# Performance work log

Hardware: AMD Instinct MI355X
Metric: run time of the kernel (lower is better)

## Reference

```python
import jax, jax.numpy as jnp
import numpy as np

N_NODES = 50000
N_EDGES = 800000
C_IN = 128
C_OUT = 64
C_HID = 2 * C_OUT  # 128


def setup_inputs() -> dict:
    key = jax.random.key(0)
    ks = jax.random.split(key, 8)
    x = jax.random.normal(ks[0], (N_NODES, C_IN), dtype=jnp.float32)
    edge_index = jax.random.randint(ks[1], (2, N_EDGES), 0, N_NODES, dtype=jnp.int64)
    s1 = 1.0 / np.sqrt(C_IN)
    s2 = 1.0 / np.sqrt(C_HID)
    s3 = 1.0 / np.sqrt(C_OUT)
    W1 = jax.random.uniform(ks[2], (C_IN, C_HID), jnp.float32, -s1, s1)
    b1 = jnp.zeros((C_HID,), jnp.float32)
    W2 = jax.random.uniform(ks[3], (C_HID, C_OUT), jnp.float32, -s2, s2)
    b2 = jnp.zeros((C_OUT,), jnp.float32)
    Wb = jax.random.uniform(ks[4], (1, C_OUT, C_OUT), jnp.float32, -s3, s3)
    bb = jax.random.uniform(ks[5], (1,), jnp.float32, -s3, s3)
    return {"x": x, "edge_index": edge_index, "W1": W1, "b1": b1,
            "W2": W2, "b2": b2, "Wb": Wb, "bb": bb}


def gcn_conv(x, W, b, src, dst, n_nodes):
    # PyG GCNConv: h = x @ W; add self-loops; symmetric normalization D^-1/2 (A+I) D^-1/2.
    h = x @ W  # [N, F]
    ones = jnp.ones((src.shape[0],), h.dtype)
    deg = jax.ops.segment_sum(ones, dst, num_segments=n_nodes) + 1.0  # +1 for self-loop
    dinv = jax.lax.rsqrt(deg)
    norm = dinv[src] * dinv[dst]  # [E]
    msgs = h[src] * norm[:, None]  # [E, F]
    agg = jax.ops.segment_sum(msgs, dst, num_segments=n_nodes)
    # self-loop contribution: norm_ii = 1/deg_i
    agg = agg + h * (1.0 / deg)[:, None]
    return agg + b


def reference(x, edge_index, W1, b1, W2, b2, Wb, bb):
    src = edge_index[0]
    dst = edge_index[1]
    n = x.shape[0]
    # encode
    h = jax.nn.relu(gcn_conv(x, W1, b1, src, dst, n))
    z = gcn_conv(h, W2, b2, src, dst, n)  # [N, C_OUT]
    # decode: bilinear on (z[src], z[dst]) -> sigmoid
    zs = z[src]  # [E, C_OUT]
    zd = z[dst]  # [E, C_OUT]
    logits = jnp.einsum('ec,ocd,ed->eo', zs, Wb, zd) + bb  # [E, 1]
    return jax.nn.sigmoid(logits)
```

## Files before the change

### kernel.cpp

```cpp
#include <hip/hip_runtime.h>
#include <hip/hip_bf16.h>


#define N_NODES 50000
#define BSH 7
#define BSZ 128
#define NBUCK ((N_NODES + BSZ - 1) / BSZ)
#define EPB 4096
#define CAP 3072
#define DSPLIT 4

typedef unsigned int u32;
typedef unsigned short u16;
typedef unsigned long long u64;

typedef __attribute__((ext_vector_type(8))) short bf16x8;
typedef __attribute__((ext_vector_type(4))) float f32x4;
union frag_u { bf16x8 f; u32 u[4]; uint4 v; };

__device__ __forceinline__ float bflo(u32 u) { return __uint_as_float(u << 16); }
__device__ __forceinline__ float bfhi(u32 u) { return __uint_as_float(u & 0xffff0000u); }
__device__ __forceinline__ u32 f2bf(float f) {
    u32 b = __float_as_uint(f);
    return (b + 0x7fffu + ((b >> 16) & 1u)) >> 16;
}
__device__ __forceinline__ u32 pack2(float a, float b) { return f2bf(a) | (f2bf(b) << 16); }

__global__ __launch_bounds__(256) void gemm1_scatter(
        const float* __restrict__ X, const float* __restrict__ W,
        u16* __restrict__ O, int n_rows, int gblk,
        const int* __restrict__ src, const int* __restrict__ dst,
        int* __restrict__ bcur, u64* __restrict__ pair, int E) {
    constexpr int K = 128, NOUT = 128;
    constexpr int KP = K + 8;
    constexpr int NT = NOUT / 16;
    constexpr int KS = K / 32;
    __shared__ __align__(16) char smem[NOUT * KP * 2 * sizeof(u16)];
    int t = threadIdx.x;

    if ((int)blockIdx.x < gblk) {
        u16* Wt_hi = (u16*)smem;
        u16* Wt_lo = Wt_hi + NOUT * KP;
        for (int i4 = t; i4 < K * NOUT / 4; i4 += 256) {
            int k = (i4 * 4) / NOUT;
            int n0 = (i4 * 4) % NOUT;
            float4 w4 = *(const float4*)&W[(size_t)k * NOUT + n0];
            float wv[4] = {w4.x, w4.y, w4.z, w4.w};
#pragma unroll
            for (int q = 0; q < 4; q++) {
                u32 hi = f2bf(wv[q]);
                u32 lo = f2bf(wv[q] - bflo(hi));
                Wt_hi[(n0 + q) * KP + k] = (u16)hi;
                Wt_lo[(n0 + q) * KP + k] = (u16)lo;
            }
        }
        __syncthreads();

        int wave = t >> 6;
        int lane = t & 63;
        int m16 = lane & 15;
        int quad = lane >> 4;
        int row0 = blockIdx.x * 128 + wave * 32;

        f32x4 acc[2][NT] = {};
        for (int ks = 0; ks < KS; ks++) {
            frag_u a_hi[2], a_lo[2];
#pragma unroll
            for (int mt = 0; mt < 2; mt++) {
                int row = row0 + mt * 16 + m16;
                row = row < n_rows ? row : n_rows - 1;
                const float* Xp = X + (size_t)row * K + ks * 32 + quad * 8;
                float4 x0 = *(const float4*)Xp;
                float4 x1 = *(const float4*)(Xp + 4);
                float xv[8] = {x0.x, x0.y, x0.z, x0.w, x1.x, x1.y, x1.z, x1.w};
#pragma unroll
                for (int p = 0; p < 4; p++) {
                    u32 h0 = f2bf(xv[2 * p]), h1 = f2bf(xv[2 * p + 1]);
                    a_hi[mt].u[p] = h0 | (h1 << 16);
                    a_lo[mt].u[p] = pack2(xv[2 * p] - bflo(h0), xv[2 * p + 1] - bflo(h1));
                }
            }
#pragma unroll
            for (int nt = 0; nt < NT; nt++) {
                int n = nt * 16 + m16;
                frag_u b_hi, b_lo;
                b_hi.v = *(const uint4*)&Wt_hi[n * KP + ks * 32 + quad * 8];
                b_lo.v = *(const uint4*)&Wt_lo[n * KP + ks * 32 + quad * 8];
#pragma unroll
                for (int mt = 0; mt < 2; mt++) {
                    acc[mt][nt] = __builtin_amdgcn_mfma_f32_16x16x32_bf16(a_hi[mt].f, b_hi.f, acc[mt][nt], 0, 0, 0);
                    acc[mt][nt] = __builtin_amdgcn_mfma_f32_16x16x32_bf16(a_hi[mt].f, b_lo.f, acc[mt][nt], 0, 0, 0);
                    acc[mt][nt] = __builtin_amdgcn_mfma_f32_16x16x32_bf16(a_lo[mt].f, b_hi.f, acc[mt][nt], 0, 0, 0);
                }
            }
        }
#pragma unroll
        for (int mt = 0; mt < 2; mt++)
#pragma unroll
            for (int nt = 0; nt < NT; nt++)
#pragma unroll
                for (int r = 0; r < 4; r++) {
                    int row = row0 + mt * 16 + quad * 4 + r;
                    if (row < n_rows)
                        O[(size_t)row * NOUT + nt * 16 + m16] = (u16)f2bf(acc[mt][nt][r]);
                }
    } else {
        int* hist = (int*)smem;
        for (int i = t; i < NBUCK; i += 256) hist[i] = 0;
        __syncthreads();
        int base = ((int)blockIdx.x - gblk) * EPB;
        int s_[16], d_[16];
#pragma unroll
        for (int it = 0; it < 16; it++) {
            int e = base + it * 256 + t;
            if (e < E) {
                s_[it] = src[e];
                d_[it] = dst[e];
                atomicAdd(&hist[d_[it] >> BSH], 1);
            } else {
                d_[it] = -1;
            }
        }
        __syncthreads();
        for (int b = t; b < NBUCK; b += 256) {
            int c = hist[b];
            hist[b] = c ? (b * CAP + atomicAdd(&bcur[b], c)) : 0;
        }
        __syncthreads();
#pragma unroll
        for (int it = 0; it < 16; it++) {
            if (d_[it] >= 0) {
                int b = d_[it] >> BSH;
                int off = atomicAdd(&hist[b], 1);
                int e = base + it * 256 + t;
                pair[off] = (u64)((u32)s_[it] | ((u32)(d_[it] & (BSZ - 1)) << 16))
                          | ((u64)(u32)e << 32);
            }
        }
    }
}

__global__ __launch_bounds__(256) void bucket_sort(u64* __restrict__ pair,
                                                   const int* __restrict__ bcur,
                                                   int* __restrict__ row_ptr,
                                                   int* __restrict__ col,
                                                   float* __restrict__ dinv,
                                                   float* __restrict__ inv, int n, int E) {
    __shared__ u64 prA[CAP];
    __shared__ u64 prB[CAP];
    __shared__ int ssum[256];
    __shared__ int histA[512];
    __shared__ int scA[512];
    __shared__ int cnt[BSZ];
    __shared__ int scn[BSZ];
    __shared__ int cur[BSZ];
    int t = threadIdx.x;
    int bucket = blockIdx.x;
    int base = bucket << BSH;
    int nn = min(BSZ, n - base);
    int accp = 0;
    for (int i = t; i < bucket; i += 256) accp += bcur[i];
    ssum[t] = accp;
    __syncthreads();
    for (int s = 128; s > 0; s >>= 1) {
        if (t < s) ssum[t] += ssum[t + s];
        __syncthreads();
    }
    int b0 = ssum[0];
    int cntE = bcur[bucket];
    int p0 = bucket * CAP;

    histA[t] = 0;
    histA[t + 256] = 0;
    __syncthreads();
    for (int j = t; j < cntE; j += 256) {
        u64 p = pair[p0 + j];
        prA[j] = p;
        atomicAdd(&histA[(int)(p & 0xffffu) >> BSH], 1);
    }
    __syncthreads();
    int h0 = histA[t], h1 = histA[t + 256];
    scA[t] = h0;
    scA[t + 256] = h1;
    __syncthreads();
    for (int off = 1; off < 512; off <<= 1) {
        int a0 = (t >= off) ? scA[t - off] : 0;
        int a1 = (t + 256 >= off) ? scA[t + 256 - off] : 0;
        __syncthreads();
        scA[t] += a0;
        scA[t + 256] += a1;
        __syncthreads();
    }
    histA[t] = scA[t] - h0;
    histA[t + 256] = scA[t + 256] - h1;
    __syncthreads();
    for (int j = t; j < cntE; j += 256) {
        u64 p = prA[j];
        int pos = atomicAdd(&histA[(int)(p & 0xffffu) >> BSH], 1);
        prB[pos] = p;
    }
    __syncthreads();
    for (int j = t; j < cntE; j += 256) pair[p0 + j] = prB[j];

    if (t < BSZ) cnt[t] = 0;
    __syncthreads();
    for (int j = t; j < cntE; j += 256)
        atomicAdd(&cnt[(int)((prB[j] >> 16) & (BSZ - 1))], 1);
    __syncthreads();
    if (t < BSZ) scn[t] = cnt[t];
    __syncthreads();
    for (int off = 1; off < BSZ; off <<= 1) {
        int a = (t < BSZ && t >= off) ? scn[t - off] : 0;
        __syncthreads();
        if (t < BSZ) scn[t] += a;
        __syncthreads();
    }
    if (t < nn) {
        int excl = b0 + scn[t] - cnt[t];
        row_ptr[base + t] = excl;
        cur[t] = excl;
        float d = (float)cnt[t] + 1.0f;
        dinv[base + t] = rsqrtf(d);
        inv[base + t] = 1.0f / d;
    }
    if (t == 0 && bucket == NBUCK - 1) row_ptr[n] = E;
    __syncthreads();
    for (int j = t; j < cntE; j += 256) {
        u64 p = prB[j];
        int ln = (int)((p >> 16) & (BSZ - 1));
        int pos = atomicAdd(&cur[ln], 1);
        col[pos] = (int)(p & 0xffffu);
    }
}

template <int K, int NOUT>
__global__ __launch_bounds__(256) void gemm_mfma_bf(const u16* __restrict__ Xv,
                                                    const float* __restrict__ W,
                                                    u16* __restrict__ O, int n_rows) {
    constexpr int KP = K + 8;
    constexpr int NT = NOUT / 16;
    constexpr int KS = K / 32;
    __shared__ __align__(16) u16 Wt_hi[NOUT * KP];
    __shared__ __align__(16) u16 Wt_lo[NOUT * KP];
    int t = threadIdx.x;
    for (int i4 = t; i4 < K * NOUT / 4; i4 += 256) {
        int k = (i4 * 4) / NOUT;
        int n0 = (i4 * 4) % NOUT;
        float4 w4 = *(const float4*)&W[(size_t)k * NOUT + n0];
        float wv[4] = {w4.x, w4.y, w4.z, w4.w};
#pragma unroll
        for (int q = 0; q < 4; q++) {
            u32 hi = f2bf(wv[q]);
            u32 lo = f2bf(wv[q] - bflo(hi));
            Wt_hi[(n0 + q) * KP + k] = (u16)hi;
            Wt_lo[(n0 + q) * KP + k] = (u16)lo;
        }
    }
    __syncthreads();

    int wave = t >> 6;
    int lane = t & 63;
    int m16 = lane & 15;
    int quad = lane >> 4;
    int row0 = blockIdx.x * 128 + wave * 32;

    f32x4 acc[2][NT] = {};
    for (int ks = 0; ks < KS; ks++) {
        frag_u a_hi[2];
#pragma unroll
        for (int mt = 0; mt < 2; mt++) {
            int row = row0 + mt * 16 + m16;
            row = row < n_rows ? row : n_rows - 1;
            a_hi[mt].v = *(const uint4*)(Xv + (size_t)row * K + ks * 32 + quad * 8);
        }
#pragma unroll
        for (int nt = 0; nt < NT; nt++) {
            int n = nt * 16 + m16;
            frag_u b_hi, b_lo;
            b_hi.v = *(const uint4*)&Wt_hi[n * KP + ks * 32 + quad * 8];
            b_lo.v = *(const uint4*)&Wt_lo[n * KP + ks * 32 + quad * 8];
#pragma unroll
            for (int mt = 0; mt < 2; mt++) {
                acc[mt][nt] = __builtin_amdgcn_mfma_f32_16x16x32_bf16(a_hi[mt].f, b_hi.f, acc[mt][nt], 0, 0, 0);
                acc[mt][nt] = __builtin_amdgcn_mfma_f32_16x16x32_bf16(a_hi[mt].f, b_lo.f, acc[mt][nt], 0, 0, 0);
            }
        }
    }
#pragma unroll
    for (int mt = 0; mt < 2; mt++)
#pragma unroll
        for (int nt = 0; nt < NT; nt++)
#pragma unroll
            for (int r = 0; r < 4; r++) {
                int row = row0 + mt * 16 + quad * 4 + r;
                if (row < n_rows)
                    O[(size_t)row * NOUT + nt * 16 + m16] = (u16)f2bf(acc[mt][nt][r]);
            }
}

template <int C, bool RELU>
__global__ __launch_bounds__(256) void agg_pull(const u16* __restrict__ H,
                                                const int* __restrict__ row_ptr,
                                                const int* __restrict__ col,
                                                const float* __restrict__ dinv,
                                                const float* __restrict__ inv,
                                                const float* __restrict__ b,
                                                u16* __restrict__ O, int n) {
    constexpr int TPN = C / 8;
    const uint4* Hv = (const uint4*)H;
    int tid = blockIdx.x * 256 + threadIdx.x;
    int node = tid / TPN;
    if (node >= n) return;
    int part = tid % TPN;
    int c8 = part * 8;
    float dn = dinv[node];
    float iv = inv[node];
    float acc[8];
    {
        uint4 h = Hv[(size_t)node * TPN + part];
        acc[0] = bflo(h.x) * iv + b[c8 + 0];
        acc[1] = bfhi(h.x) * iv + b[c8 + 1];
        acc[2] = bflo(h.y) * iv + b[c8 + 2];
        acc[3] = bfhi(h.y) * iv + b[c8 + 3];
        acc[4] = bflo(h.z) * iv + b[c8 + 4];
        acc[5] = bfhi(h.z) * iv + b[c8 + 5];
        acc[6] = bflo(h.w) * iv + b[c8 + 6];
        acc[7] = bfhi(h.w) * iv + b[c8 + 7];
    }
    int j = row_ptr[node];
    int end = row_ptr[node + 1];
    for (; j + 7 < end; j += 8) {
        int s0 = col[j],     s1 = col[j + 1], s2 = col[j + 2], s3 = col[j + 3];
        int s4 = col[j + 4], s5 = col[j + 5], s6 = col[j + 6], s7 = col[j + 7];
        float n0 = dn * dinv[s0], n1 = dn * dinv[s1];
        float n2 = dn * dinv[s2], n3 = dn * dinv[s3];
        float n4 = dn * dinv[s4], n5 = dn * dinv[s5];
        float n6 = dn * dinv[s6], n7 = dn * dinv[s7];
        uint4 v0 = Hv[(size_t)s0 * TPN + part];
        uint4 v1 = Hv[(size_t)s1 * TPN + part];
        uint4 v2 = Hv[(size_t)s2 * TPN + part];
        uint4 v3 = Hv[(size_t)s3 * TPN + part];
        uint4 v4 = Hv[(size_t)s4 * TPN + part];
        uint4 v5 = Hv[(size_t)s5 * TPN + part];
        uint4 v6 = Hv[(size_t)s6 * TPN + part];
        uint4 v7 = Hv[(size_t)s7 * TPN + part];
        acc[0] += bflo(v0.x) * n0 + bflo(v1.x) * n1 + bflo(v2.x) * n2 + bflo(v3.x) * n3;
        acc[1] += bfhi(v0.x) * n0 + bfhi(v1.x) * n1 + bfhi(v2.x) * n2 + bfhi(v3.x) * n3;
        acc[2] += bflo(v0.y) * n0 + bflo(v1.y) * n1 + bflo(v2.y) * n2 + bflo(v3.y) * n3;
        acc[3] += bfhi(v0.y) * n0 + bfhi(v1.y) * n1 + bfhi(v2.y) * n2 + bfhi(v3.y) * n3;
        acc[4] += bflo(v0.z) * n0 + bflo(v1.z) * n1 + bflo(v2.z) * n2 + bflo(v3.z) * n3;
        acc[5] += bfhi(v0.z) * n0 + bfhi(v1.z) * n1 + bfhi(v2.z) * n2 + bfhi(v3.z) * n3;
        acc[6] += bflo(v0.w) * n0 + bflo(v1.w) * n1 + bflo(v2.w) * n2 + bflo(v3.w) * n3;
        acc[7] += bfhi(v0.w) * n0 + bfhi(v1.w) * n1 + bfhi(v2.w) * n2 + bfhi(v3.w) * n3;
        acc[0] += bflo(v4.x) * n4 + bflo(v5.x) * n5 + bflo(v6.x) * n6 + bflo(v7.x) * n7;
        acc[1] += bfhi(v4.x) * n4 + bfhi(v5.x) * n5 + bfhi(v6.x) * n6 + bfhi(v7.x) * n7;
        acc[2] += bflo(v4.y) * n4 + bflo(v5.y) * n5 + bflo(v6.y) * n6 + bflo(v7.y) * n7;
        acc[3] += bfhi(v4.y) * n4 + bfhi(v5.y) * n5 + bfhi(v6.y) * n6 + bfhi(v7.y) * n7;
        acc[4] += bflo(v4.z) * n4 + bflo(v5.z) * n5 + bflo(v6.z) * n6 + bflo(v7.z) * n7;
        acc[5] += bfhi(v4.z) * n4 + bfhi(v5.z) * n5 + bfhi(v6.z) * n6 + bfhi(v7.z) * n7;
        acc[6] += bflo(v4.w) * n4 + bflo(v5.w) * n5 + bflo(v6.w) * n6 + bflo(v7.w) * n7;
        acc[7] += bfhi(v4.w) * n4 + bfhi(v5.w) * n5 + bfhi(v6.w) * n6 + bfhi(v7.w) * n7;
    }
    for (; j + 3 < end; j += 4) {
        int s0 = col[j], s1 = col[j + 1], s2 = col[j + 2], s3 = col[j + 3];
        float n0 = dn * dinv[s0], n1 = dn * dinv[s1];
        float n2 = dn * dinv[s2], n3 = dn * dinv[s3];
        uint4 v0 = Hv[(size_t)s0 * TPN + part];
        uint4 v1 = Hv[(size_t)s1 * TPN + part];
        uint4 v2 = Hv[(size_t)s2 * TPN + part];
        uint4 v3 = Hv[(size_t)s3 * TPN + part];
        acc[0] += bflo(v0.x) * n0 + bflo(v1.x) * n1 + bflo(v2.x) * n2 + bflo(v3.x) * n3;
        acc[1] += bfhi(v0.x) * n0 + bfhi(v1.x) * n1 + bfhi(v2.x) * n2 + bfhi(v3.x) * n3;
        acc[2] += bflo(v0.y) * n0 + bflo(v1.y) * n1 + bflo(v2.y) * n2 + bflo(v3.y) * n3;
        acc[3] += bfhi(v0.y) * n0 + bfhi(v1.y) * n1 + bfhi(v2.y) * n2 + bfhi(v3.y) * n3;
        acc[4] += bflo(v0.z) * n0 + bflo(v1.z) * n1 + bflo(v2.z) * n2 + bflo(v3.z) * n3;
        acc[5] += bfhi(v0.z) * n0 + bfhi(v1.z) * n1 + bfhi(v2.z) * n2 + bfhi(v3.z) * n3;
        acc[6] += bflo(v0.w) * n0 + bflo(v1.w) * n1 + bflo(v2.w) * n2 + bflo(v3.w) * n3;
        acc[7] += bfhi(v0.w) * n0 + bfhi(v1.w) * n1 + bfhi(v2.w) * n2 + bfhi(v3.w) * n3;
    }
    for (; j < end; j++) {
        int s = col[j];
        float nm = dn * dinv[s];
        uint4 v = Hv[(size_t)s * TPN + part];
        acc[0] += bflo(v.x) * nm; acc[1] += bfhi(v.x) * nm;
        acc[2] += bflo(v.y) * nm; acc[3] += bfhi(v.y) * nm;
        acc[4] += bflo(v.z) * nm; acc[5] += bfhi(v.z) * nm;
        acc[6] += bflo(v.w) * nm; acc[7] += bfhi(v.w) * nm;
    }
    if (RELU) {
#pragma unroll
        for (int i = 0; i < 8; i++) acc[i] = fmaxf(acc[i], 0.f);
    }
    uint4 o;
    o.x = pack2(acc[0], acc[1]);
    o.y = pack2(acc[2], acc[3]);
    o.z = pack2(acc[4], acc[5]);
    o.w = pack2(acc[6], acc[7]);
    ((uint4*)O)[(size_t)node * TPN + part] = o;
}

__global__ __launch_bounds__(256) void decode_fused(const u16* __restrict__ Z,
                                                    const float* __restrict__ Wb,
                                                    const u64* __restrict__ pair,
                                                    const int* __restrict__ bcur,
                                                    const float* __restrict__ bb,
                                                    float* __restrict__ out, int n) {
    constexpr int K = 64, NOUT = 64;
    constexpr int KP = K + 8;
    constexpr int QP = 72;
    __shared__ __align__(16) u16 Wt_hi[NOUT * KP];
    __shared__ __align__(16) u16 Wt_lo[NOUT * KP];
    __shared__ __align__(16) u16 Qs[BSZ * QP];
    int t = threadIdx.x;
    int bucket = blockIdx.x / DSPLIT;
    int part = blockIdx.x % DSPLIT;
    int base = bucket << BSH;

    for (int i4 = t; i4 < K * NOUT / 4; i4 += 256) {
        int nn_ = (i4 * 4) / K;
        int k0 = (i4 * 4) % K;
        float4 w4 = *(const float4*)&Wb[(size_t)nn_ * K + k0];
        float wv[4] = {w4.x, w4.y, w4.z, w4.w};
#pragma unroll
        for (int q = 0; q < 4; q++) {
            u32 hi = f2bf(wv[q]);
            u32 lo = f2bf(wv[q] - bflo(hi));
            Wt_hi[nn_ * KP + k0 + q] = (u16)hi;
            Wt_lo[nn_ * KP + k0 + q] = (u16)lo;
        }
    }
    __syncthreads();

    {
        int wave = t >> 6;
        int lane = t & 63;
        int m16 = lane & 15;
        int quad = lane >> 4;
        int row0 = wave * 32;
        f32x4 acc[2][4] = {};
        for (int ks = 0; ks < 2; ks++) {
            frag_u a[2];
#pragma unroll
            for (int mt = 0; mt < 2; mt++) {
                int node = base + row0 + mt * 16 + m16;
                node = node < n ? node : n - 1;
                a[mt].v = *(const uint4*)(Z + (size_t)node * K + ks * 32 + quad * 8);
            }
#pragma unroll
            for (int nt = 0; nt < 4; nt++) {
                int nc = nt * 16 + m16;
                frag_u b_hi, b_lo;
                b_hi.v = *(const uint4*)&Wt_hi[nc * KP + ks * 32 + quad * 8];
                b_lo.v = *(const uint4*)&Wt_lo[nc * KP + ks * 32 + quad * 8];
#pragma unroll
                for (int mt = 0; mt < 2; mt++) {
                    acc[mt][nt] = __builtin_amdgcn_mfma_f32_16x16x32_bf16(a[mt].f, b_hi.f, acc[mt][nt], 0, 0, 0);
                    acc[mt][nt] = __builtin_amdgcn_mfma_f32_16x16x32_bf16(a[mt].f, b_lo.f, acc[mt][nt], 0, 0, 0);
                }
            }
        }
#pragma unroll
        for (int mt = 0; mt < 2; mt++)
#pragma unroll
            for (int nt = 0; nt < 4; nt++)
#pragma unroll
                for (int r = 0; r < 4; r++) {
                    int rl = row0 + mt * 16 + quad * 4 + r;
                    Qs[rl * QP + nt * 16 + m16] = (u16)f2bf(acc[mt][nt][r]);
                }
    }
    __syncthreads();

    const uint4* Zv = (const uint4*)Z;
    int cntE = bcur[bucket];
    int p0 = bucket * CAP;
    int chunk = (cntE + DSPLIT - 1) / DSPLIT;
    int s0 = part * chunk;
    int s1 = min(s0 + chunk, cntE);
    float bbv = bb[0];
    int lane8 = t & 7;
    int grp = t >> 3;
    for (int j = s0 + grp * 2; j < s1; j += 64) {
        u64 pA = pair[p0 + j];
        bool has2 = (j + 1) < s1;
        u64 pB = has2 ? pair[p0 + j + 1] : pA;
        int sA = (int)(pA & 0xffffu);
        int sB = (int)(pB & 0xffffu);
        int locA = (int)((pA >> 16) & (BSZ - 1));
        int locB = (int)((pB >> 16) & (BSZ - 1));
        uint4 zA = Zv[(size_t)sA * 8 + lane8];
        uint4 zB = Zv[(size_t)sB * 8 + lane8];
        uint4 qA = *(const uint4*)&Qs[locA * QP + lane8 * 8];
        uint4 qB = *(const uint4*)&Qs[locB * QP + lane8 * 8];
        float dA = bflo(zA.x) * bflo(qA.x) + bfhi(zA.x) * bfhi(qA.x)
                 + bflo(zA.y) * bflo(qA.y) + bfhi(zA.y) * bfhi(qA.y)
                 + bflo(zA.z) * bflo(qA.z) + bfhi(zA.z) * bfhi(qA.z)
                 + bflo(zA.w) * bflo(qA.w) + bfhi(zA.w) * bfhi(qA.w);
        float dB = bflo(zB.x) * bflo(qB.x) + bfhi(zB.x) * bfhi(qB.x)
                 + bflo(zB.y) * bflo(qB.y) + bfhi(zB.y) * bfhi(qB.y)
                 + bflo(zB.z) * bflo(qB.z) + bfhi(zB.z) * bfhi(qB.z)
                 + bflo(zB.w) * bflo(qB.w) + bfhi(zB.w) * bfhi(qB.w);
        dA += __shfl_down(dA, 4, 8);
        dA += __shfl_down(dA, 2, 8);
        dA += __shfl_down(dA, 1, 8);
        dB += __shfl_down(dB, 4, 8);
        dB += __shfl_down(dB, 2, 8);
        dB += __shfl_down(dB, 1, 8);
        if (lane8 == 0) {
            out[(int)(pA >> 32)] = 1.0f / (1.0f + expf(-(dA + bbv)));
            if (has2) out[(int)(pB >> 32)] = 1.0f / (1.0f + expf(-(dB + bbv)));
        }
    }
}

extern "C" void kernel_launch(void* const* d_in, const int* in_sizes, int n_in,
                              void* d_out, int out_size, void* d_ws, size_t ws_size,
                              hipStream_t stream) {
    const float* x  = (const float*)d_in[0];
    const int*   ei = (const int*)d_in[1];
    const float* W1 = (const float*)d_in[2];
    const float* b1 = (const float*)d_in[3];
    const float* W2 = (const float*)d_in[4];
    const float* b2 = (const float*)d_in[5];
    const float* Wb = (const float*)d_in[6];
    const float* bb = (const float*)d_in[7];
    float* out = (float*)d_out;

    const int N = N_NODES;
    const int E = in_sizes[1] / 2;
    const int* src = ei;
    const int* dst = ei + E;
    const int GBLK = (N + 127) / 128;
    const int SBLK = (E + EPB - 1) / EPB;

    char* w = (char*)d_ws;
    int*   bcur    = (int*)w;   w += (size_t)512 * 4;
    int*   row_ptr = (int*)w;   w += (size_t)(N + 1) * 4;
    int*   col     = (int*)w;   w += (size_t)E * 4;
    w = (char*)(((size_t)w + 15) & ~(size_t)15);
    u64*   pair    = (u64*)w;   w += (size_t)NBUCK * CAP * 8;
    float* dinv    = (float*)w; w += (size_t)N * 4;
    float* inv     = (float*)w; w += (size_t)N * 4;
    w = (char*)(((size_t)w + 15) & ~(size_t)15);
    u16* bufA = (u16*)w;        w += (size_t)N * 128 * 2;
    u16* bufB = (u16*)w;        w += (size_t)N * 128 * 2;
    u16* bufC = (u16*)w;

    u16* H1 = bufA;
    u16* h1 = bufB;
    u16* H2 = bufA;
    u16* Z  = bufC;

    hipMemsetAsync(bcur, 0, 512 * 4, stream);
    gemm1_scatter<<<GBLK + SBLK, 256, 0, stream>>>(x, W1, H1, N, GBLK,
                                                   src, dst, bcur, pair, E);
    bucket_sort<<<NBUCK, 256, 0, stream>>>(pair, bcur, row_ptr, col, dinv, inv, N, E);

    agg_pull<128, true><<<((size_t)N * 16 + 255) / 256, 256, 0, stream>>>(
        H1, row_ptr, col, dinv, inv, b1, h1, N);

    gemm_mfma_bf<128, 64><<<GBLK, 256, 0, stream>>>(h1, W2, H2, N);
    agg_pull<64, false><<<((size_t)N * 8 + 255) / 256, 256, 0, stream>>>(
        H2, row_ptr, col, dinv, inv, b2, Z, N);

    decode_fused<<<NBUCK * DSPLIT, 256, 0, stream>>>(Z, Wb, pair, bcur, bb, out, N);
}
```

Before: 223.7 us.

## Phase neighbor gathers by source-index range with block barriers for cache locality

The pull aggregation now splits each node's sorted neighbor list into PH source-index ranges and processes them in phases, with a block-wide barrier between phases. All threads in a block therefore gather from roughly the same slice of H at the same time, which is meant to raise L2/MALL hit rates for the random gathers. Inactive threads stay alive so they can take part in the barriers. The cost is a linear scan to find each phase boundary, plus barriers that make whole blocks wait on their slowest node. The scheme only helps if col is sorted by source within each row.

```diff
diff --git a/kernel.cpp b/kernel.cpp
--- a/kernel.cpp
+++ b/kernel.cpp
@@ -298,7 +298,7 @@
             }
 }
 
-template <int C, bool RELU>
+template <int C, bool RELU, int PH>
 __global__ __launch_bounds__(256) void agg_pull(const u16* __restrict__ H,
                                                 const int* __restrict__ row_ptr,
                                                 const int* __restrict__ col,
@@ -310,13 +310,15 @@
     const uint4* Hv = (const uint4*)H;
     int tid = blockIdx.x * 256 + threadIdx.x;
     int node = tid / TPN;
-    if (node >= n) return;
+    bool act = node < n;
     int part = tid % TPN;
     int c8 = part * 8;
-    float dn = dinv[node];
-    float iv = inv[node];
-    float acc[8];
-    {
+    float dn = 0.f, iv = 0.f;
+    float acc[8] = {};
+    int j = 0, end = 0;
+    if (act) {
+        dn = dinv[node];
+        iv = inv[node];
         uint4 h = Hv[(size_t)node * TPN + part];
         acc[0] = bflo(h.x) * iv + b[c8 + 0];
         acc[1] = bfhi(h.x) * iv + b[c8 + 1];
@@ -326,67 +328,79 @@
         acc[5] = bfhi(h.z) * iv + b[c8 + 5];
         acc[6] = bflo(h.w) * iv + b[c8 + 6];
         acc[7] = bfhi(h.w) * iv + b[c8 + 7];
-    }
-    int j = row_ptr[node];
-    int end = row_ptr[node + 1];
-    for (; j + 7 < end; j += 8) {
-        int s0 = col[j],     s1 = col[j + 1], s2 = col[j + 2], s3 = col[j + 3];
-        int s4 = col[j + 4], s5 = col[j + 5], s6 = col[j + 6], s7 = col[j + 7];
-        float n0 = dn * dinv[s0], n1 = dn * dinv[s1];
-        float n2 = dn * dinv[s2], n3 = dn * dinv[s3];
-        float n4 = dn * dinv[s4], n5 = dn * dinv[s5];
-        float n6 = dn * dinv[s6], n7 = dn * dinv[s7];
-        uint4 v0 = Hv[(size_t)s0 * TPN + part];
-        uint4 v1 = Hv[(size_t)s1 * TPN + part];
-        uint4 v2 = Hv[(size_t)s2 * TPN + part];
-        uint4 v3 = Hv[(size_t)s3 * TPN + part];
-        uint4 v4 = Hv[(size_t)s4 * TPN + part];
-        uint4 v5 = Hv[(size_t)s5 * TPN + part];
-        uint4 v6 = Hv[(size_t)s6 * TPN + part];
-        uint4 v7 = Hv[(size_t)s7 * TPN + part];
-        acc[0] += bflo(v0.x) * n0 + bflo(v1.x) * n1 + bflo(v2.x) * n2 + bflo(v3.x) * n3;
-        acc[1] += bfhi(v0.x) * n0 + bfhi(v1.x) * n1 + bfhi(v2.x) * n2 + bfhi(v3.x) * n3;
-        acc[2] += bflo(v0.y) * n0 + bflo(v1.y) * n1 + bflo(v2.y) * n2 + bflo(v3.y) * n3;
-        acc[3] += bfhi(v0.y) * n0 + bfhi(v1.y) * n1 + bfhi(v2.y) * n2 + bfhi(v3.y) * n3;
-        acc[4] += bflo(v0.z) * n0 + bflo(v1.z) * n1 + bflo(v2.z) * n2 + bflo(v3.z) * n3;
-        acc[5] += bfhi(v0.z) * n0 + bfhi(v1.z) * n1 + bfhi(v2.z) * n2 + bfhi(v3.z) * n3;
-        acc[6] += bflo(v0.w) * n0 + bflo(v1.w) * n1 + bflo(v2.w) * n2 + bflo(v3.w) * n3;
-        acc[7] += bfhi(v0.w) * n0 + bfhi(v1.w) * n1 + bfhi(v2.w) * n2 + bfhi(v3.w) * n3;
-        acc[0] += bflo(v4.x) * n4 + bflo(v5.x) * n5 + bflo(v6.x) * n6 + bflo(v7.x) * n7;
-        acc[1] += bfhi(v4.x) * n4 + bfhi(v5.x) * n5 + bfhi(v6.x) * n6 + bfhi(v7.x) * n7;
-        acc[2] += bflo(v4.y) * n4 + bflo(v5.y) * n5 + bflo(v6.y) * n6 + bflo(v7.y) * n7;
-        acc[3] += bfhi(v4.y) * n4 + bfhi(v5.y) * n5 + bfhi(v6.y) * n6 + bfhi(v7.y) * n7;
-        acc[4] += bflo(v4.z) * n4 + bflo(v5.z) * n5 + bflo(v6.z) * n6 + bflo(v7.z) * n7;
-        acc[5] += bfhi(v4.z) * n4 + bfhi(v5.z) * n5 + bfhi(v6.z) * n6 + bfhi(v7.z) * n7;
-        acc[6] += bflo(v4.w) * n4 + bflo(v5.w) * n5 + bflo(v6.w) * n6 + bflo(v7.w) * n7;
-        acc[7] += bfhi(v4.w) * n4 + bfhi(v5.w) * n5 + bfhi(v6.w) * n6 + bfhi(v7.w) * n7;
-    }
-    for (; j + 3 < end; j += 4) {
-        int s0 = col[j], s1 = col[j + 1], s2 = col[j + 2], s3 = col[j + 3];
-        float n0 = dn * dinv[s0], n1 = dn * dinv[s1];
-        float n2 = dn * dinv[s2], n3 = dn * dinv[s3];
-        uint4 v0 = Hv[(size_t)s0 * TPN + part];
-        uint4 v1 = Hv[(size_t)s1 * TPN + part];
-        uint4 v2 = Hv[(size_t)s2 * TPN + part];
-        uint4 v3 = Hv[(size_t)s3 * TPN + part];
-        acc[0] += bflo(v0.x) * n0 + bflo(v1.x) * n1 + bflo(v2.x) * n2 + bflo(v3.x) * n3;
-        acc[1] += bfhi(v0.x) * n0 + bfhi(v1.x) * n1 + bfhi(v2.x) * n2 + bfhi(v3.x) * n3;
-        acc[2] += bflo(v0.y) * n0 + bflo(v1.y) * n1 + bflo(v2.y) * n2 + bflo(v3.y) * n3;
-        acc[3] += bfhi(v0.y) * n0 + bfhi(v1.y) * n1 + bfhi(v2.y) * n2 + bfhi(v3.y) * n3;
-        acc[4] += bflo(v0.z) * n0 + bflo(v1.z) * n1 + bflo(v2.z) * n2 + bflo(v3.z) * n3;
-        acc[5] += bfhi(v0.z) * n0 + bfhi(v1.z) * n1 + bfhi(v2.z) * n2 + bfhi(v3.z) * n3;
-        acc[6] += bflo(v0.w) * n0 + bflo(v1.w) * n1 + bflo(v2.w) * n2 + bflo(v3.w) * n3;
-        acc[7] += bfhi(v0.w) * n0 + bfhi(v1.w) * n1 + bfhi(v2.w) * n2 + bfhi(v3.w) * n3;
-    }
-    for (; j < end; j++) {
-        int s = col[j];
-        float nm = dn * dinv[s];
-        uint4 v = Hv[(size_t)s * TPN + part];
-        acc[0] += bflo(v.x) * nm; acc[1] += bfhi(v.x) * nm;
-        acc[2] += bflo(v.y) * nm; acc[3] += bfhi(v.y) * nm;
-        acc[4] += bflo(v.z) * nm; acc[5] += bfhi(v.z) * nm;
-        acc[6] += bflo(v.w) * nm; acc[7] += bfhi(v.w) * nm;
-    }
+        j = row_ptr[node];
+        end = row_ptr[node + 1];
+    }
+    const int wstep = (n + PH - 1) / PH;
+#pragma unroll 1
+    for (int ph = 1; ph <= PH; ph++) {
+        int e2 = end;
+        if (ph < PH) {
+            int bound = ph * wstep;
+            e2 = j;
+            while (e2 < end && col[e2] < bound) e2++;
+        }
+        for (; j + 7 < e2; j += 8) {
+            int s0 = col[j],     s1 = col[j + 1], s2 = col[j + 2], s3 = col[j + 3];
+            int s4 = col[j + 4], s5 = col[j + 5], s6 = col[j + 6], s7 = col[j + 7];
+            float n0 = dn * dinv[s0], n1 = dn * dinv[s1];
+            float n2 = dn * dinv[s2], n3 = dn * dinv[s3];
+            float n4 = dn * dinv[s4], n5 = dn * dinv[s5];
+            float n6 = dn * dinv[s6], n7 = dn * dinv[s7];
+            uint4 v0 = Hv[(size_t)s0 * TPN + part];
+            uint4 v1 = Hv[(size_t)s1 * TPN + part];
+            uint4 v2 = Hv[(size_t)s2 * TPN + part];
+            uint4 v3 = Hv[(size_t)s3 * TPN + part];
+            uint4 v4 = Hv[(size_t)s4 * TPN + part];
+            uint4 v5 = Hv[(size_t)s5 * TPN + part];
+            uint4 v6 = Hv[(size_t)s6 * TPN + part];
+            uint4 v7 = Hv[(size_t)s7 * TPN + part];
+            acc[0] += bflo(v0.x) * n0 + bflo(v1.x) * n1 + bflo(v2.x) * n2 + bflo(v3.x) * n3;
+            acc[1] += bfhi(v0.x) * n0 + bfhi(v1.x) * n1 + bfhi(v2.x) * n2 + bfhi(v3.x) * n3;
+            acc[2] += bflo(v0.y) * n0 + bflo(v1.y) * n1 + bflo(v2.y) * n2 + bflo(v3.y) * n3;
+            acc[3] += bfhi(v0.y) * n0 + bfhi(v1.y) * n1 + bfhi(v2.y) * n2 + bfhi(v3.y) * n3;
+            acc[4] += bflo(v0.z) * n0 + bflo(v1.z) * n1 + bflo(v2.z) * n2 + bflo(v3.z) * n3;
+            acc[5] += bfhi(v0.z) * n0 + bfhi(v1.z) * n1 + bfhi(v2.z) * n2 + bfhi(v3.z) * n3;
+            acc[6] += bflo(v0.w) * n0 + bflo(v1.w) * n1 + bflo(v2.w) * n2 + bflo(v3.w) * n3;
+            acc[7] += bfhi(v0.w) * n0 + bfhi(v1.w) * n1 + bfhi(v2.w) * n2 + bfhi(v3.w) * n3;
+            acc[0] += bflo(v4.x) * n4 + bflo(v5.x) * n5 + bflo(v6.x) * n6 + bflo(v7.x) * n7;
+            acc[1] += bfhi(v4.x) * n4 + bfhi(v5.x) * n5 + bfhi(v6.x) * n6 + bfhi(v7.x) * n7;
+            acc[2] += bflo(v4.y) * n4 + bflo(v5.y) * n5 + bflo(v6.y) * n6 + bflo(v7.y) * n7;
+            acc[3] += bfhi(v4.y) * n4 + bfhi(v5.y) * n5 + bfhi(v6.y) * n6 + bfhi(v7.y) * n7;
+            acc[4] += bflo(v4.z) * n4 + bflo(v5.z) * n5 + bflo(v6.z) * n6 + bflo(v7.z) * n7;
+            acc[5] += bfhi(v4.z) * n4 + bfhi(v5.z) * n5 + bfhi(v6.z) * n6 + bfhi(v7.z) * n7;
+            acc[6] += bflo(v4.w) * n4 + bflo(v5.w) * n5 + bflo(v6.w) * n6 + bflo(v7.w) * n7;
+            acc[7] += bfhi(v4.w) * n4 + bfhi(v5.w) * n5 + bfhi(v6.w) * n6 + bfhi(v7.w) * n7;
+        }
+        for (; j + 3 < e2; j += 4) {
+            int s0 = col[j], s1 = col[j + 1], s2 = col[j + 2], s3 = col[j + 3];
+            float n0 = dn * dinv[s0], n1 = dn * dinv[s1];
+            float n2 = dn * dinv[s2], n3 = dn * dinv[s3];
+            uint4 v0 = Hv[(size_t)s0 * TPN + part];
+            uint4 v1 = Hv[(size_t)s1 * TPN + part];
+            uint4 v2 = Hv[(size_t)s2 * TPN + part];
+            uint4 v3 = Hv[(size_t)s3 * TPN + part];
+            acc[0] += bflo(v0.x) * n0 + bflo(v1.x) * n1 + bflo(v2.x) * n2 + bflo(v3.x) * n3;
+            acc[1] += bfhi(v0.x) * n0 + bfhi(v1.x) * n1 + bfhi(v2.x) * n2 + bfhi(v3.x) * n3;
+            acc[2] += bflo(v0.y) * n0 + bflo(v1.y) * n1 + bflo(v2.y) * n2 + bflo(v3.y) * n3;
+            acc[3] += bfhi(v0.y) * n0 + bfhi(v1.y) * n1 + bfhi(v2.y) * n2 + bfhi(v3.y) * n3;
+            acc[4] += bflo(v0.z) * n0 + bflo(v1.z) * n1 + bflo(v2.z) * n2 + bflo(v3.z) * n3;
+            acc[5] += bfhi(v0.z) * n0 + bfhi(v1.z) * n1 + bfhi(v2.z) * n2 + bfhi(v3.z) * n3;
+            acc[6] += bflo(v0.w) * n0 + bflo(v1.w) * n1 + bflo(v2.w) * n2 + bflo(v3.w) * n3;
+            acc[7] += bfhi(v0.w) * n0 + bfhi(v1.w) * n1 + bfhi(v2.w) * n2 + bfhi(v3.w) * n3;
+        }
+        for (; j < e2; j++) {
+            int s = col[j];
+            float nm = dn * dinv[s];
+            uint4 v = Hv[(size_t)s * TPN + part];
+            acc[0] += bflo(v.x) * nm; acc[1] += bfhi(v.x) * nm;
+            acc[2] += bflo(v.y) * nm; acc[3] += bfhi(v.y) * nm;
+            acc[4] += bflo(v.z) * nm; acc[5] += bfhi(v.z) * nm;
+            acc[6] += bflo(v.w) * nm; acc[7] += bfhi(v.w) * nm;
+        }
+        if (ph < PH) __syncthreads();
+    }
+    if (!act) return;
     if (RELU) {
 #pragma unroll
         for (int i = 0; i < 8; i++) acc[i] = fmaxf(acc[i], 0.f);
@@ -556,11 +570,11 @@
                                                    src, dst, bcur, pair, E);
     bucket_sort<<<NBUCK, 256, 0, stream>>>(pair, bcur, row_ptr, col, dinv, inv, N, E);
 
-    agg_pull<128, true><<<((size_t)N * 16 + 255) / 256, 256, 0, stream>>>(
+    agg_pull<128, true, 4><<<((size_t)N * 16 + 255) / 256, 256, 0, stream>>>(
         H1, row_ptr, col, dinv, inv, b1, h1, N);
 
     gemm_mfma_bf<128, 64><<<GBLK, 256, 0, stream>>>(h1, W2, H2, N);
-    agg_pull<64, false><<<((size_t)N * 8 + 255) / 256, 256, 0, stream>>>(
+    agg_pull<64, false, 2><<<((size_t)N * 8 + 255) / 256, 256, 0, stream>>>(
         H2, row_ptr, col, dinv, inv, b2, Z, N);
 
     decode_fused<<<NBUCK * DSPLIT, 256, 0, stream>>>(Z, Wb, pair, bcur, bb, out, N);
```

Measured after the change: 273.8 us. +22.4%, slower.
